# Optimization experiments

Measured on AMD Instinct MI355X. Metric: run time of the kernel, lower is better.

Reference implementation:

```python
import jax, jax.numpy as jnp
import numpy as np

WINDOW_SIZE = 7
C1 = 0.01 ** 2
C2 = 0.03 ** 2


def _gaussian_window(ws: int) -> jnp.ndarray:
    sigma = ws / 6.0
    coords = jnp.arange(ws, dtype=jnp.float32) - ws // 2
    g = jnp.exp(-coords ** 2 / (2 * sigma ** 2))
    g = g / g.sum()
    k3 = g[:, None, None] * g[None, :, None] * g[None, None, :]
    k3 = k3 / k3.sum()
    return k3.reshape(1, 1, ws, ws, ws)  # OIDHW


def _conv3d_same(x, w):
    pad = WINDOW_SIZE // 2
    return jax.lax.conv_general_dilated(
        x, w, window_strides=(1, 1, 1),
        padding=[(pad, pad)] * 3,
        dimension_numbers=('NCDHW', 'OIDHW', 'NCDHW'))


def setup_inputs() -> dict:
    key = jax.random.key(0)
    k1, k2 = jax.random.split(key)
    shape = (2, 1, 160, 160, 160)
    predicted = jax.random.uniform(k1, shape, dtype=jnp.float32)
    target = jax.random.uniform(k2, shape, dtype=jnp.float32)
    return {"predicted": predicted, "target": target}


def reference(predicted, target):
    window = _gaussian_window(WINDOW_SIZE)
    mu1 = _conv3d_same(predicted, window)
    mu2 = _conv3d_same(target, window)
    mu1_sq = mu1 ** 2
    mu2_sq = mu2 ** 2
    mu1_mu2 = mu1 * mu2
    sigma1_sq = _conv3d_same(predicted ** 2, window) - mu1_sq
    sigma2_sq = _conv3d_same(target ** 2, window) - mu2_sq
    sigma12 = _conv3d_same(predicted * target, window) - mu1_mu2
    ssim_map = ((2 * mu1_mu2 + C1) * (2 * sigma12 + C2)) / (
        (mu1_sq + mu2_sq + C1) * (sigma1_sq + sigma2_sq + C2))
    return 1.0 - ssim_map.mean()
```

## Files before the change

kernel.cpp:

```cpp
#include <hip/hip_runtime.h>
#include <math.h>

#define DD 160
#define HH 160
#define WW 160
#define NB 2
#define NEL (NB*DD*HH*WW)

#define XT 32
#define YT 16
#define ZC 16
#define NTHR 256
#define NZCH (DD/ZC)
#define GX (WW/XT)
#define GY (HH/YT)
#define NPART (GX*GY*NB*NZCH)

#define PCOLS 38
#define HR 22
#define PPITCH 42
#define CPITCH 33

struct G7 { float g[7]; };

__device__ __forceinline__ float2 f2fma(float s, float2 a, float2 b) {
    return make_float2(fmaf(s, a.x, b.x), fmaf(s, a.y, b.y));
}

__global__ __launch_bounds__(NTHR, 4) void ssim_fused(
        const float* __restrict__ p, const float* __restrict__ t,
        float* __restrict__ partial, G7 gw) {
    const int tid = threadIdx.x;
    const int tx  = tid & 31;
    const int tyo = tid >> 5;
    const int x0 = blockIdx.x * XT;
    const int y0 = blockIdx.y * YT;
    const int n  = blockIdx.z / NZCH;
    const int zs = (blockIdx.z % NZCH) * ZC;

    __shared__ float2 spt[HR][PPITCH];
    __shared__ float2 squ[HR][PPITCH];
    __shared__ float4 c4[HR][CPITCH];

    float2 r01[2][6], r23[2][6];
#pragma unroll
    for (int yo = 0; yo < 2; ++yo)
#pragma unroll
        for (int j = 0; j < 6; ++j) {
            r01[yo][j] = make_float2(0.f, 0.f);
            r23[yo][j] = make_float2(0.f, 0.f);
        }

    const float C1v = 1e-4f, C2v = 9e-4f;
    float ssum = 0.f;
    const int hw = HH * WW;
    const float* pv = p + (size_t)n * DD * hw;
    const float* tv = t + (size_t)n * DD * hw;

    for (int s = zs - 3; s < zs + ZC + 3; ++s) {
        float2 m01[2], m23[2];
#pragma unroll
        for (int yo = 0; yo < 2; ++yo) {
            m01[yo] = make_float2(0.f, 0.f);
            m23[yo] = make_float2(0.f, 0.f);
        }

        const bool valid = (s >= 0) && (s < DD);
        if (valid) {
            const float* pb = pv + (size_t)s * hw;
            const float* tb = tv + (size_t)s * hw;

            for (int i = tid; i < PCOLS * HR; i += NTHR) {
                int r = i / PCOLS, c = i - r * PCOLS;
                int gy = y0 + r - 3, gx = x0 + c - 3;
                float a = 0.f, b = 0.f;
                if ((unsigned)gy < (unsigned)HH && (unsigned)gx < (unsigned)WW) {
                    a = pb[gy * WW + gx];
                    b = tb[gy * WW + gx];
                }
                float u = a + b, d = a - b;
                spt[r][c] = make_float2(a, b);
                squ[r][c] = make_float2(u * u, d * d);
            }
            __syncthreads();

            if (tid < HR * 8) {
                int r = tid >> 3, xg = tid & 7;
                const float4* P4 = (const float4*)&spt[r][0];
                const float4* Q4 = (const float4*)&squ[r][0];
                float2 pt[10], qu[10];
#pragma unroll
                for (int k = 0; k < 5; ++k) {
                    float4 a = P4[2 * xg + k];
                    pt[2 * k]     = make_float2(a.x, a.y);
                    pt[2 * k + 1] = make_float2(a.z, a.w);
                    float4 b = Q4[2 * xg + k];
                    qu[2 * k]     = make_float2(b.x, b.y);
                    qu[2 * k + 1] = make_float2(b.z, b.w);
                }
#pragma unroll
                for (int e = 0; e < 4; ++e) {
                    float2 s01 = make_float2(0.f, 0.f);
                    float2 s23 = make_float2(0.f, 0.f);
#pragma unroll
                    for (int k = 0; k < 7; ++k) {
                        float w = gw.g[k];
                        s01 = f2fma(w, pt[e + k], s01);
                        s23 = f2fma(w, qu[e + k], s23);
                    }
                    c4[r][4 * xg + e] = make_float4(s01.x, s01.y, s23.x, s23.y);
                }
            }
            __syncthreads();

#pragma unroll
            for (int r8 = 0; r8 < 8; ++r8) {
                float4 v = c4[2 * tyo + r8][tx];
                float2 v01 = make_float2(v.x, v.y);
                float2 v23 = make_float2(v.z, v.w);
                if (r8 < 7) {
                    float w = gw.g[r8];
                    m01[0] = f2fma(w, v01, m01[0]);
                    m23[0] = f2fma(w, v23, m23[0]);
                }
                if (r8 > 0) {
                    float w = gw.g[r8 - 1];
                    m01[1] = f2fma(w, v01, m01[1]);
                    m23[1] = f2fma(w, v23, m23[1]);
                }
            }
        }

        float2 cons01[2], cons23[2];
#pragma unroll
        for (int yo = 0; yo < 2; ++yo) {
            float2 v01 = m01[yo], v23 = m23[yo];
            cons01[yo] = f2fma(gw.g[6], v01, r01[yo][0]);
            cons23[yo] = f2fma(gw.g[6], v23, r23[yo][0]);
#pragma unroll
            for (int j = 0; j < 5; ++j) {
                r01[yo][j] = f2fma(gw.g[5 - j], v01, r01[yo][j + 1]);
                r23[yo][j] = f2fma(gw.g[5 - j], v23, r23[yo][j + 1]);
            }
            r01[yo][5] = make_float2(gw.g[0] * v01.x, gw.g[0] * v01.y);
            r23[yo][5] = make_float2(gw.g[0] * v23.x, gw.g[0] * v23.y);
        }

        if (s >= zs + 3) {
#pragma unroll
            for (int yo = 0; yo < 2; ++yo) {
                float mu1 = cons01[yo].x, mu2 = cons01[yo].y;
                float Eu  = cons23[yo].x, Ew  = cons23[yo].y;
                float mu12 = mu1 * mu2, mu1sq = mu1 * mu1, mu2sq = mu2 * mu2;
                float sumsq = 0.5f  * (Eu + Ew) - mu1sq - mu2sq;
                float s12   = 0.25f * (Eu - Ew) - mu12;
                float num = (2.f * mu12 + C1v) * (2.f * s12 + C2v);
                float den = (mu1sq + mu2sq + C1v) * (sumsq + C2v);
                ssum += num * __builtin_amdgcn_rcpf(den);
            }
        }
    }

#pragma unroll
    for (int off = 32; off > 0; off >>= 1)
        ssum += __shfl_down(ssum, off, 64);
    __shared__ float wsum[4];
    if ((tid & 63) == 0) wsum[tid >> 6] = ssum;
    __syncthreads();
    if (tid == 0) {
        int bid = (blockIdx.z * GY + blockIdx.y) * GX + blockIdx.x;
        partial[bid] = wsum[0] + wsum[1] + wsum[2] + wsum[3];
    }
}

__global__ __launch_bounds__(256) void ssim_final(
        const float* __restrict__ partial, float* __restrict__ out) {
    float s = 0.f;
    for (int i = threadIdx.x; i < NPART; i += 256) s += partial[i];
#pragma unroll
    for (int off = 32; off > 0; off >>= 1)
        s += __shfl_down(s, off, 64);
    __shared__ float wsum[4];
    int lane = threadIdx.x & 63, wid = threadIdx.x >> 6;
    if (lane == 0) wsum[wid] = s;
    __syncthreads();
    if (threadIdx.x == 0) {
        float tot = wsum[0] + wsum[1] + wsum[2] + wsum[3];
        out[0] = 1.0f - tot / (float)NEL;
    }
}

extern "C" void kernel_launch(void* const* d_in, const int* in_sizes, int n_in,
                              void* d_out, int out_size, void* d_ws, size_t ws_size,
                              hipStream_t stream) {
    const float* p = (const float*)d_in[0];
    const float* t = (const float*)d_in[1];
    float* out = (float*)d_out;
    float* partial = (float*)d_ws;

    G7 gw;
    {
        double s = 0.0, sig = 7.0 / 6.0;
        double g[7];
        for (int i = 0; i < 7; ++i) {
            double d = (double)i - 3.0;
            g[i] = exp(-d * d / (2.0 * sig * sig));
            s += g[i];
        }
        for (int i = 0; i < 7; ++i) gw.g[i] = (float)(g[i] / s);
    }

    dim3 grid(GX, GY, NB * NZCH);
    ssim_fused<<<grid, NTHR, 0, stream>>>(p, t, partial, gw);
    ssim_final<<<1, 256, 0, stream>>>(partial, out);
}
```

Before: 153.2 us.

## Load rows directly into registers and double-buffer column-filtered smem tile

Removes the raw and squared-input shared-memory staging. Each of the 176 filter threads now reads its 12 input columns with float4 global loads, forms the products in registers, and runs the horizontal pass directly. The intermediate tile is double-buffered by slice parity, which drops one __syncthreads per slice, and it is padded to cut bank conflicts. In exchange only 176 of 256 threads issue global loads, and adjacent threads load overlapping columns, so global traffic per thread goes up.

```diff
diff --git a/kernel.cpp b/kernel.cpp
--- a/kernel.cpp
+++ b/kernel.cpp
@@ -16,10 +16,8 @@
 #define GY (HH/YT)
 #define NPART (GX*GY*NB*NZCH)
 
-#define PCOLS 38
 #define HR 22
-#define PPITCH 42
-#define CPITCH 33
+#define CP 35
 
 struct G7 { float g[7]; };
 
@@ -38,9 +36,7 @@
     const int n  = blockIdx.z / NZCH;
     const int zs = (blockIdx.z % NZCH) * ZC;
 
-    __shared__ float2 spt[HR][PPITCH];
-    __shared__ float2 squ[HR][PPITCH];
-    __shared__ float4 c4[HR][CPITCH];
+    __shared__ float4 c4[2][HR][CP];
 
     float2 r01[2][6], r23[2][6];
 #pragma unroll
@@ -57,7 +53,15 @@
     const float* pv = p + (size_t)n * DD * hw;
     const float* tv = t + (size_t)n * DD * hw;
 
+    const int br = tid >> 3;
+    const int bxg = tid & 7;
+    const int bgy = y0 + br - 3;
+    const bool browok = (unsigned)bgy < (unsigned)HH && tid < HR * 8;
+    const int cbase = x0 + 4 * bxg - 4;
+    const int pcr = tx + (tx >> 3);
+
     for (int s = zs - 3; s < zs + ZC + 3; ++s) {
+        const int par = s & 1;
         float2 m01[2], m23[2];
 #pragma unroll
         for (int yo = 0; yo < 2; ++yo) {
@@ -67,36 +71,32 @@
 
         const bool valid = (s >= 0) && (s < DD);
         if (valid) {
-            const float* pb = pv + (size_t)s * hw;
-            const float* tb = tv + (size_t)s * hw;
-
-            for (int i = tid; i < PCOLS * HR; i += NTHR) {
-                int r = i / PCOLS, c = i - r * PCOLS;
-                int gy = y0 + r - 3, gx = x0 + c - 3;
-                float a = 0.f, b = 0.f;
-                if ((unsigned)gy < (unsigned)HH && (unsigned)gx < (unsigned)WW) {
-                    a = pb[gy * WW + gx];
-                    b = tb[gy * WW + gx];
-                }
-                float u = a + b, d = a - b;
-                spt[r][c] = make_float2(a, b);
-                squ[r][c] = make_float2(u * u, d * d);
-            }
-            __syncthreads();
-
             if (tid < HR * 8) {
-                int r = tid >> 3, xg = tid & 7;
-                const float4* P4 = (const float4*)&spt[r][0];
-                const float4* Q4 = (const float4*)&squ[r][0];
-                float2 pt[10], qu[10];
-#pragma unroll
-                for (int k = 0; k < 5; ++k) {
-                    float4 a = P4[2 * xg + k];
-                    pt[2 * k]     = make_float2(a.x, a.y);
-                    pt[2 * k + 1] = make_float2(a.z, a.w);
-                    float4 b = Q4[2 * xg + k];
-                    qu[2 * k]     = make_float2(b.x, b.y);
-                    qu[2 * k + 1] = make_float2(b.z, b.w);
+                const float* prow = pv + (size_t)s * hw + bgy * WW;
+                const float* trow = tv + (size_t)s * hw + bgy * WW;
+                float2 pt[12], qu[12];
+#pragma unroll
+                for (int q = 0; q < 3; ++q) {
+                    int c0 = cbase + 4 * q;
+                    float4 a = make_float4(0.f, 0.f, 0.f, 0.f);
+                    float4 b = a;
+                    if (browok && (unsigned)c0 < (unsigned)WW) {
+                        a = *(const float4*)(prow + c0);
+                        b = *(const float4*)(trow + c0);
+                    }
+                    float u, d;
+                    pt[4*q+0] = make_float2(a.x, b.x);
+                    u = a.x + b.x; d = a.x - b.x;
+                    qu[4*q+0] = make_float2(u * u, d * d);
+                    pt[4*q+1] = make_float2(a.y, b.y);
+                    u = a.y + b.y; d = a.y - b.y;
+                    qu[4*q+1] = make_float2(u * u, d * d);
+                    pt[4*q+2] = make_float2(a.z, b.z);
+                    u = a.z + b.z; d = a.z - b.z;
+                    qu[4*q+2] = make_float2(u * u, d * d);
+                    pt[4*q+3] = make_float2(a.w, b.w);
+                    u = a.w + b.w; d = a.w - b.w;
+                    qu[4*q+3] = make_float2(u * u, d * d);
                 }
 #pragma unroll
                 for (int e = 0; e < 4; ++e) {
@@ -105,17 +105,19 @@
 #pragma unroll
                     for (int k = 0; k < 7; ++k) {
                         float w = gw.g[k];
-                        s01 = f2fma(w, pt[e + k], s01);
-                        s23 = f2fma(w, qu[e + k], s23);
+                        s01 = f2fma(w, pt[e + k + 1], s01);
+                        s23 = f2fma(w, qu[e + k + 1], s23);
                     }
-                    c4[r][4 * xg + e] = make_float4(s01.x, s01.y, s23.x, s23.y);
+                    int c = 4 * bxg + e;
+                    c4[par][br][c + (c >> 3)] =
+                        make_float4(s01.x, s01.y, s23.x, s23.y);
                 }
             }
             __syncthreads();
 
 #pragma unroll
             for (int r8 = 0; r8 < 8; ++r8) {
-                float4 v = c4[2 * tyo + r8][tx];
+                float4 v = c4[par][2 * tyo + r8][pcr];
                 float2 v01 = make_float2(v.x, v.y);
                 float2 v23 = make_float2(v.z, v.w);
                 if (r8 < 7) {
```

Measured after the change: 136.2 us. -11.1%, faster.
